# Kernel tuning notes

Measured on AMD Instinct MI355X. Metric: run time of the kernel, lower is better.

Reference implementation:

```python
import jax, jax.numpy as jnp
import numpy as np

B, S, D, H, DH = 2, 1024, 1024, 16, 64  # batch, seq, dim_model, heads, dim_head


def setup_inputs() -> dict:
    key = jax.random.key(0)
    ks = jax.random.split(key, 9)
    def W(k):
        return jax.random.normal(k, (D, D), jnp.float32) * 0.02
    z = jnp.zeros((D,), jnp.float32)
    return {
        "x": jax.random.normal(ks[0], (B, S, D), jnp.float32),
        "rel_pos_emb": jax.random.normal(ks[1], (B, S, D), jnp.float32),
        "padding_mask": jnp.zeros((B, S), jnp.int32),
        "Wq": W(ks[2]), "bq": z,
        "Wk": W(ks[3]), "bk": z,
        "Wv": W(ks[4]), "bv": z,
        "Wqr": W(ks[5]), "bqr": z,
        "Wkr": W(ks[6]), "bkr": z,
        "Wc": W(ks[7]), "bc": z,
    }


def reference(x, rel_pos_emb, padding_mask, Wq, bq, Wk, bk, Wv, bv, Wqr, bqr, Wkr, bkr, Wc, bc):
    b, s, d = x.shape

    def proj(t, W_, b_):  # (b,s,D) -> (b,H,s,DH)
        return (t @ W_.T + b_).reshape(b, s, H, DH).transpose(0, 2, 1, 3)

    q = proj(x, Wq, bq)
    k = proj(x, Wk, bk)
    v = proj(x, Wv, bv)
    qr = proj(rel_pos_emb, Wqr, bqr)
    kr = proj(rel_pos_emb, Wkr, bkr)

    # relative position index: clamp(i - j + MAX_REL_POS/2, 0, MAX_REL_POS-1), MAX_REL_POS = S
    idx = jnp.arange(s)
    pos = jnp.clip(idx[:, None] - idx[None, :] + s // 2, 0, s - 1)  # (s,s) int
    pos_b = jnp.broadcast_to(pos[None, None], (b, H, s, s))

    c2c = jnp.einsum('bhid,bhjd->bhij', q, k)
    c2p_att = jnp.einsum('bhid,bhjd->bhij', q, kr)
    c2p = jnp.take_along_axis(c2p_att, pos_b, axis=-1)   # gather along last dim
    p2c_att = jnp.einsum('bhid,bhjd->bhij', qr, k)
    p2c = jnp.take_along_axis(p2c_att, pos_b, axis=-2)   # gather along query dim

    scale = jnp.sqrt(jnp.asarray(3 * DH, jnp.float32))
    scores = (c2c + c2p + p2c) / scale
    scores = jnp.where(padding_mask[:, None, None, :] == 1, -jnp.inf, scores)
    attn = jax.nn.softmax(scores, axis=-1)  # dropout is identity in eval

    out = jnp.einsum('bhij,bhjd->bhid', attn, v)
    out = out.transpose(0, 2, 1, 3).reshape(b, s, H * DH)
    return out @ Wc.T + bc
```

## Files before the change

### kernel.cpp

```cpp
#include <hip/hip_runtime.h>

typedef unsigned short u16;
typedef unsigned int   u32;
typedef __bf16 bf16x8 __attribute__((ext_vector_type(8)));
typedef float  f32x4  __attribute__((ext_vector_type(4)));

__device__ __forceinline__ float b2f(u16 s) { return __uint_as_float(((u32)s) << 16); }
__device__ __forceinline__ u16 f2b(float f) {
  u32 x = __float_as_uint(f);
  return (u16)((x + 0x7FFFu + ((x >> 16) & 1u)) >> 16);
}

union U16x8 { uint4 u; u16 s[8]; };

__device__ __forceinline__ uint4 cvt8(const float4 a, const float4 b) {
  U16x8 r;
  r.s[0] = f2b(a.x); r.s[1] = f2b(a.y); r.s[2] = f2b(a.z); r.s[3] = f2b(a.w);
  r.s[4] = f2b(b.x); r.s[5] = f2b(b.y); r.s[6] = f2b(b.z); r.s[7] = f2b(b.w);
  return r.u;
}

typedef __attribute__((address_space(3))) u32 lds_u32;
typedef const __attribute__((address_space(1))) u32 glb_u32;
__device__ __forceinline__ void gld16(const u16* gp, u16* lp) {
  __builtin_amdgcn_global_load_lds((glb_u32*)gp, (lds_u32*)lp, 16, 0, 0);
}

struct CvtArgs { const float* s[8]; u16* d[8]; int n[8]; };

__global__ __launch_bounds__(256) void cvt_bf16(CvtArgs c) {
  const int t = blockIdx.y;
  const int i = (blockIdx.x * 256 + threadIdx.x) * 8;
  if (i >= c.n[t]) return;
  const float4 a = *(const float4*)(c.s[t] + i);
  const float4 b = *(const float4*)(c.s[t] + i + 4);
  *(uint4*)(c.d[t] + i) = cvt8(a, b);
}

struct GemmBArgs { const u16* A[5]; const u16* W[5]; const float* Bi[5]; void* C[5]; int vtz; };

template <int BN, bool OUT_F32>
__global__ __launch_bounds__(256) void gemm_lds(GemmBArgs g, int M, int N, int K) {
  const int z = blockIdx.z;
  const u16* __restrict__ A = g.A[z];
  const u16* __restrict__ W = g.W[z];
  const float* __restrict__ Bi = g.Bi[z];

  const int m0 = blockIdx.y * 128, n0 = blockIdx.x * BN;
  const int tid = threadIdx.x, wv = tid >> 6, lane = tid & 63;
  const int wm = wv >> 1, wn = wv & 1;
  const int lr = lane & 15, lq = lane >> 4;
  constexpr int NT = BN / 32;

  __shared__ u16 As[128 * 64];
  __shared__ u16 Ws[BN * 64];

  const f32x4 vzero = {0.f, 0.f, 0.f, 0.f};
  f32x4 acc[4][NT];
#pragma unroll
  for (int i = 0; i < 4; ++i)
#pragma unroll
    for (int j = 0; j < NT; ++j) acc[i][j] = vzero;

  const int srow = lane >> 3;
  const int sc   = (lane & 7) ^ srow;

  for (int kb = 0; kb < K; kb += 64) {
    __syncthreads();
#pragma unroll
    for (int t = 0; t < 4; ++t) {
      const u16* gp = A + (size_t)(m0 + t * 32 + wv * 8 + srow) * K + kb + sc * 8;
      gld16(gp, As + (t * 32 + wv * 8) * 64 + lane * 8);
    }
#pragma unroll
    for (int t = 0; t < NT; ++t) {
      const u16* gp = W + (size_t)(n0 + t * 32 + wv * 8 + srow) * K + kb + sc * 8;
      gld16(gp, Ws + (t * 32 + wv * 8) * 64 + lane * 8);
    }
    __syncthreads();
#pragma unroll
    for (int kk = 0; kk < 2; ++kk) {
      bf16x8 af[4], bw[NT];
#pragma unroll
      for (int mt = 0; mt < 4; ++mt) {
        const int row = wm * 64 + mt * 16 + lr;
        af[mt] = *(const bf16x8*)&As[row * 64 + (((kk << 2) | lq) ^ (row & 7)) * 8];
      }
#pragma unroll
      for (int nt = 0; nt < NT; ++nt) {
        const int row = wn * (BN / 2) + nt * 16 + lr;
        bw[nt] = *(const bf16x8*)&Ws[row * 64 + (((kk << 2) | lq) ^ (row & 7)) * 8];
      }
#pragma unroll
      for (int mt = 0; mt < 4; ++mt)
#pragma unroll
        for (int nt = 0; nt < NT; ++nt)
          acc[mt][nt] = __builtin_amdgcn_mfma_f32_16x16x32_bf16(af[mt], bw[nt], acc[mt][nt], 0, 0, 0);
    }
  }

#pragma unroll
  for (int mt = 0; mt < 4; ++mt) {
#pragma unroll
    for (int nt = 0; nt < NT; ++nt) {
      const int col = n0 + wn * (BN / 2) + nt * 16 + lr;
      const float bia = Bi[col];
      const int row0 = m0 + wm * 64 + mt * 16 + lq * 4;
      if (OUT_F32) {
#pragma unroll
        for (int r = 0; r < 4; ++r)
          ((float*)g.C[z])[(size_t)(row0 + r) * N + col] = acc[mt][nt][r] + bia;
      } else if (z == g.vtz) {
        ushort4 pk;
        pk.x = f2b(acc[mt][nt][0] + bia); pk.y = f2b(acc[mt][nt][1] + bia);
        pk.z = f2b(acc[mt][nt][2] + bia); pk.w = f2b(acc[mt][nt][3] + bia);
        const int bb = row0 >> 10, s0 = row0 & 1023;
        *(ushort4*)((u16*)g.C[z] + ((size_t)bb << 20) + ((size_t)col << 10) + s0) = pk;
      } else {
#pragma unroll
        for (int r = 0; r < 4; ++r)
          ((u16*)g.C[z])[(size_t)(row0 + r) * N + col] = f2b(acc[mt][nt][r] + bia);
      }
    }
  }
}

struct GemmArgs { const void* A[5]; const float* W[5]; const float* Bi[5]; void* C[5]; int vtz; };

template <bool A_F32, bool OUT_F32>
__global__ __launch_bounds__(256) void gemm5(GemmArgs g, int M, int N, int K) {
  const int z = blockIdx.z;
  const float* __restrict__ Wf = g.W[z];
  const float* __restrict__ Bi = g.Bi[z];

  const int m0 = blockIdx.y * 128, n0 = blockIdx.x * 128;
  const int tid = threadIdx.x;
  const int wv = tid >> 6, lane = tid & 63;
  const int wm = wv >> 1, wn = wv & 1;
  const int lr = lane & 15, lq = lane >> 4;

  __shared__ alignas(16) u16 As[128][64];
  __shared__ alignas(16) u16 Ws[128][64];

  const f32x4 vzero = {0.f, 0.f, 0.f, 0.f};
  f32x4 acc[4][4];
#pragma unroll
  for (int i = 0; i < 4; ++i)
#pragma unroll
    for (int j = 0; j < 4; ++j) acc[i][j] = vzero;

  const int srow = tid >> 1;
  const int sc0  = (tid & 1) * 32;
  const float* pw = Wf + (size_t)(n0 + srow) * K + sc0;
  const float* paf = A_F32 ? ((const float*)g.A[z] + (size_t)(m0 + srow) * K + sc0) : nullptr;
  const u16*   pab = A_F32 ? nullptr : ((const u16*)g.A[z] + (size_t)(m0 + srow) * K + sc0);

  for (int k0 = 0; k0 < K; k0 += 64) {
#pragma unroll
    for (int u_ = 0; u_ < 4; ++u_) {
      const float4 w0 = *(const float4*)(pw + k0 + u_ * 8);
      const float4 w1 = *(const float4*)(pw + k0 + u_ * 8 + 4);
      *(uint4*)&Ws[srow][sc0 + u_ * 8] = cvt8(w0, w1);
      if (A_F32) {
        const float4 a0 = *(const float4*)(paf + k0 + u_ * 8);
        const float4 a1 = *(const float4*)(paf + k0 + u_ * 8 + 4);
        *(uint4*)&As[srow][sc0 + u_ * 8] = cvt8(a0, a1);
      } else {
        *(uint4*)&As[srow][sc0 + u_ * 8] = *(const uint4*)(pab + k0 + u_ * 8);
      }
    }
    __syncthreads();
#pragma unroll
    for (int kk = 0; kk < 2; ++kk) {
      bf16x8 af[4], bfr[4];
#pragma unroll
      for (int mt = 0; mt < 4; ++mt)
        af[mt] = *(const bf16x8*)&As[wm * 64 + mt * 16 + lr][kk * 32 + lq * 8];
#pragma unroll
      for (int nt = 0; nt < 4; ++nt)
        bfr[nt] = *(const bf16x8*)&Ws[wn * 64 + nt * 16 + lr][kk * 32 + lq * 8];
#pragma unroll
      for (int mt = 0; mt < 4; ++mt)
#pragma unroll
        for (int nt = 0; nt < 4; ++nt)
          acc[mt][nt] = __builtin_amdgcn_mfma_f32_16x16x32_bf16(af[mt], bfr[nt], acc[mt][nt], 0, 0, 0);
    }
    __syncthreads();
  }

#pragma unroll
  for (int mt = 0; mt < 4; ++mt) {
#pragma unroll
    for (int nt = 0; nt < 4; ++nt) {
      const int col = n0 + wn * 64 + nt * 16 + lr;
      const float bia = Bi[col];
      const int row0 = m0 + wm * 64 + mt * 16 + lq * 4;
      if (OUT_F32) {
#pragma unroll
        for (int r = 0; r < 4; ++r)
          ((float*)g.C[z])[(size_t)(row0 + r) * N + col] = acc[mt][nt][r] + bia;
      } else if (z == g.vtz) {
        ushort4 pk;
        pk.x = f2b(acc[mt][nt][0] + bia); pk.y = f2b(acc[mt][nt][1] + bia);
        pk.z = f2b(acc[mt][nt][2] + bia); pk.w = f2b(acc[mt][nt][3] + bia);
        const int bb = row0 >> 10, s0 = row0 & 1023;
        *(ushort4*)((u16*)g.C[z] + ((size_t)bb << 20) + ((size_t)col << 10) + s0) = pk;
      } else {
#pragma unroll
        for (int r = 0; r < 4; ++r)
          ((u16*)g.C[z])[(size_t)(row0 + r) * N + col] = f2b(acc[mt][nt][r] + bia);
      }
    }
  }
}

__global__ __launch_bounds__(256) void attn_fused(
    const u16* __restrict__ q, const u16* __restrict__ k,
    const u16* __restrict__ vT, const u16* __restrict__ qr,
    const u16* __restrict__ kr, const int* __restrict__ pmask,
    u16* __restrict__ ao) {
  constexpr int S = 1024, Dm = 1024;

  const int bx = blockIdx.x;
  const int bh = bx & 31, it = bx >> 5;
  const int bb = bh >> 4, h = bh & 15;
  const int i0 = it * 32;

  const int tid = threadIdx.x;
  const int wv = tid >> 6, lane = tid & 63;
  const int wm = wv >> 1, wn = wv & 1;
  const int lr = lane & 15, lq = lane >> 4;

  __shared__ alignas(16) u16 Qs[32][72];
  __shared__ alignas(16) u16 Ks[32][72];
  __shared__ alignas(16) u16 Vt[64][40];
  __shared__ alignas(16) u16 KRw[64][72];
  __shared__ alignas(16) u16 QRw[64][72];
  __shared__ alignas(16) float Sc[32][36];
  __shared__ alignas(16) u16 M1s[32][68];
  __shared__ alignas(16) u16 M2s[64][36];
  __shared__ alignas(16) u16 Pb[32][40];
  __shared__ float mrow[32], lrow_[32], arow[32];
  __shared__ int maskj[32];

  const size_t hoff = (size_t)h * 64;
  const u16* qb  = q  + (size_t)bb * S * Dm + hoff;
  const u16* kb  = k  + (size_t)bb * S * Dm + hoff;
  const u16* vtb = vT + ((size_t)bb << 20) + ((size_t)h << 16);
  const u16* qrb = qr + (size_t)bb * S * Dm + hoff;
  const u16* krb = kr + (size_t)bb * S * Dm + hoff;

  if (tid < 32) { mrow[tid] = -1e30f; lrow_[tid] = 0.f; }
  {
    const int a = tid >> 3, seg = (tid & 7) * 8;
    *(uint4*)&Qs[a][seg] = *(const uint4*)(qb + (size_t)(i0 + a) * Dm + seg);
  }

  const f32x4 vzero = {0.f, 0.f, 0.f, 0.f};
  f32x4 oacc[2] = {vzero, vzero};
  const float kscale = 1.44269504088896f / 13.856406460551018f;

#pragma unroll 1
  for (int jt = 0; jt < 32; ++jt) {
    const int j0 = jt * 32;
    const int pb_ = i0 - j0 + 481;
    __syncthreads();

    {
      const int jj = tid >> 3, d0 = (tid & 7) * 8;
      *(uint4*)&Ks[jj][d0] = *(const uint4*)(kb + (size_t)(j0 + jj) * Dm + d0);
      const int d = tid >> 2, jseg = (tid & 3) * 8;
      *(uint4*)&Vt[d][jseg] = *(const uint4*)(vtb + ((size_t)d << 10) + j0 + jseg);
    }
    {
      const int trow = tid >> 2, sg = (tid & 3) * 16;
      int p = pb_ + trow; p = p < 0 ? 0 : (p > 1023 ? 1023 : p);
      const u16* krp = krb + (size_t)p * Dm + sg;
      const u16* qrp = qrb + (size_t)p * Dm + sg;
      *(uint4*)&KRw[trow][sg]     = *(const uint4*)krp;
      *(uint4*)&KRw[trow][sg + 8] = *(const uint4*)(krp + 8);
      *(uint4*)&QRw[trow][sg]     = *(const uint4*)qrp;
      *(uint4*)&QRw[trow][sg + 8] = *(const uint4*)(qrp + 8);
    }
    if (tid < 32) maskj[tid] = pmask[(size_t)bb * S + j0 + tid];
    __syncthreads();

    bf16x8 aq[2], bkf[2];
#pragma unroll
    for (int kk = 0; kk < 2; ++kk) {
      aq[kk]  = *(const bf16x8*)&Qs[wm * 16 + lr][kk * 32 + lq * 8];
      bkf[kk] = *(const bf16x8*)&Ks[wn * 16 + lr][kk * 32 + lq * 8];
    }
    {
      f32x4 cc = vzero;
      cc = __builtin_amdgcn_mfma_f32_16x16x32_bf16(aq[0], bkf[0], cc, 0, 0, 0);
      cc = __builtin_amdgcn_mfma_f32_16x16x32_bf16(aq[1], bkf[1], cc, 0, 0, 0);
#pragma unroll
      for (int r = 0; r < 4; ++r) Sc[wm * 16 + lq * 4 + r][wn * 16 + lr] = cc[r];
    }
#pragma unroll
    for (int nti = 0; nti < 2; ++nti) {
      const int nt = wn + nti * 2;
      f32x4 m1 = vzero;
#pragma unroll
      for (int kk = 0; kk < 2; ++kk) {
        bf16x8 bkr8 = *(const bf16x8*)&KRw[nt * 16 + lr][kk * 32 + lq * 8];
        m1 = __builtin_amdgcn_mfma_f32_16x16x32_bf16(aq[kk], bkr8, m1, 0, 0, 0);
      }
#pragma unroll
      for (int r = 0; r < 4; ++r) M1s[wm * 16 + lq * 4 + r][nt * 16 + lr] = f2b(m1[r]);
    }
#pragma unroll
    for (int mti = 0; mti < 2; ++mti) {
      const int mt = wm + mti * 2;
      f32x4 m2 = vzero;
#pragma unroll
      for (int kk = 0; kk < 2; ++kk) {
        bf16x8 aqr8 = *(const bf16x8*)&QRw[mt * 16 + lr][kk * 32 + lq * 8];
        m2 = __builtin_amdgcn_mfma_f32_16x16x32_bf16(aqr8, bkf[kk], m2, 0, 0, 0);
      }
#pragma unroll
      for (int r = 0; r < 4; ++r) M2s[mt * 16 + lq * 4 + r][wn * 16 + lr] = f2b(m2[r]);
    }
    __syncthreads();

    {
      const int a_ = tid >> 3;
      const int b0 = (tid & 7) * 4;
      const float4 sc4 = *(const float4*)&Sc[a_][b0];
      float sv[4];
      sv[0] = sc4.x; sv[1] = sc4.y; sv[2] = sc4.z; sv[3] = sc4.w;
#pragma unroll
      for (int xq = 0; xq < 4; ++xq) {
        const int b_ = b0 + xq;
        const int tI = a_ - b_ + 31;
        const float scv = sv[xq] + b2f(M1s[a_][tI]) + b2f(M2s[tI][b_]);
        sv[xq] = maskj[b_] ? -1e30f : scv * kscale;
      }
      float mx = fmaxf(fmaxf(sv[0], sv[1]), fmaxf(sv[2], sv[3]));
      mx = fmaxf(mx, __shfl_xor(mx, 1));
      mx = fmaxf(mx, __shfl_xor(mx, 2));
      mx = fmaxf(mx, __shfl_xor(mx, 4));
      const float mold = mrow[a_];
      const float mnew = fmaxf(mold, mx);
      float ls = 0.f;
      u32 pk[2];
#pragma unroll
      for (int xq = 0; xq < 2; ++xq) {
        const float p0 = exp2f(sv[2 * xq] - mnew);
        const float p1 = exp2f(sv[2 * xq + 1] - mnew);
        ls += p0 + p1;
        pk[xq] = (u32)f2b(p0) | ((u32)f2b(p1) << 16);
      }
      ls += __shfl_xor(ls, 1);
      ls += __shfl_xor(ls, 2);
      ls += __shfl_xor(ls, 4);
      if ((tid & 7) == 0) {
        const float al = exp2f(mold - mnew);
        mrow[a_] = mnew;
        lrow_[a_] = lrow_[a_] * al + ls;
        arow[a_] = al;
      }
      *(u32*)&Pb[a_][b0]     = pk[0];
      *(u32*)&Pb[a_][b0 + 2] = pk[1];
    }
    __syncthreads();

    {
      float alph[4];
#pragma unroll
      for (int r = 0; r < 4; ++r) alph[r] = arow[wm * 16 + lq * 4 + r];
#pragma unroll
      for (int t2 = 0; t2 < 2; ++t2)
#pragma unroll
        for (int r = 0; r < 4; ++r) oacc[t2][r] *= alph[r];
      bf16x8 ap = *(const bf16x8*)&Pb[wm * 16 + lr][lq * 8];
#pragma unroll
      for (int nti = 0; nti < 2; ++nti) {
        const int nt = wn + nti * 2;
        bf16x8 bv8 = *(const bf16x8*)&Vt[nt * 16 + lr][lq * 8];
        oacc[nti] = __builtin_amdgcn_mfma_f32_16x16x32_bf16(ap, bv8, oacc[nti], 0, 0, 0);
      }
    }
  }

#pragma unroll
  for (int nti = 0; nti < 2; ++nti) {
    const int nt = wn + nti * 2;
#pragma unroll
    for (int r = 0; r < 4; ++r) {
      const int rl = wm * 16 + lq * 4 + r;
      const float ov = oacc[nti][r] / lrow_[rl];
      ao[((size_t)bb * S + i0 + rl) * Dm + hoff + nt * 16 + lr] = f2b(ov);
    }
  }
}

extern "C" void kernel_launch(void* const* d_in, const int* in_sizes, int n_in,
                              void* d_out, int out_size, void* d_ws, size_t ws_size,
                              hipStream_t stream) {
  const float* x   = (const float*)d_in[0];
  const float* rpe = (const float*)d_in[1];
  const int*   pm  = (const int*)d_in[2];
  const float* Wq  = (const float*)d_in[3];  const float* bq  = (const float*)d_in[4];
  const float* Wk  = (const float*)d_in[5];  const float* bk  = (const float*)d_in[6];
  const float* Wv  = (const float*)d_in[7];  const float* bv  = (const float*)d_in[8];
  const float* Wqr = (const float*)d_in[9];  const float* bqr = (const float*)d_in[10];
  const float* Wkr = (const float*)d_in[11]; const float* bkr = (const float*)d_in[12];
  const float* Wc  = (const float*)d_in[13]; const float* bc  = (const float*)d_in[14];

  const size_t NE = (size_t)2 * 1024 * 1024;
  const size_t WE = (size_t)1024 * 1024;
  u16* ws = (u16*)d_ws;

  if (ws_size >= (10 * NE + 6 * WE) * sizeof(u16)) {
    u16* q   = ws;          u16* k   = ws + NE;     u16* vT  = ws + 2 * NE;
    u16* qr  = ws + 3 * NE; u16* kr  = ws + 4 * NE;
    u16* xb  = ws + 5 * NE;
    u16* ao  = ws + 5 * NE;
    u16* rpb = ws + 6 * NE;
    u16* wb  = ws + 7 * NE;
    u16* Wqb = wb;           u16* Wkb = wb + WE;     u16* Wvb = wb + 2 * WE;
    u16* Wqrb= wb + 3 * WE;  u16* Wkrb= wb + 4 * WE; u16* Wcb = wb + 5 * WE;

    CvtArgs c;
    c.s[0] = x;   c.d[0] = xb;   c.n[0] = (int)NE;
    c.s[1] = rpe; c.d[1] = rpb;  c.n[1] = (int)NE;
    c.s[2] = Wq;  c.d[2] = Wqb;  c.n[2] = (int)WE;
    c.s[3] = Wk;  c.d[3] = Wkb;  c.n[3] = (int)WE;
    c.s[4] = Wv;  c.d[4] = Wvb;  c.n[4] = (int)WE;
    c.s[5] = Wqr; c.d[5] = Wqrb; c.n[5] = (int)WE;
    c.s[6] = Wkr; c.d[6] = Wkrb; c.n[6] = (int)WE;
    c.s[7] = Wc;  c.d[7] = Wcb;  c.n[7] = (int)WE;
    cvt_bf16<<<dim3(1024, 8), 256, 0, stream>>>(c);

    GemmBArgs g;
    g.A[0] = xb;  g.W[0] = Wqb;  g.Bi[0] = bq;  g.C[0] = q;
    g.A[1] = xb;  g.W[1] = Wkb;  g.Bi[1] = bk;  g.C[1] = k;
    g.A[2] = xb;  g.W[2] = Wvb;  g.Bi[2] = bv;  g.C[2] = vT;
    g.A[3] = rpb; g.W[3] = Wqrb; g.Bi[3] = bqr; g.C[3] = qr;
    g.A[4] = rpb; g.W[4] = Wkrb; g.Bi[4] = bkr; g.C[4] = kr;
    g.vtz = 2;
    gemm_lds<128, false><<<dim3(8, 16, 5), 256, 0, stream>>>(g, 2048, 1024, 1024);

    attn_fused<<<dim3(1024), 256, 0, stream>>>(q, k, vT, qr, kr, pm, ao);

    GemmBArgs g2;
    for (int i = 0; i < 5; ++i) { g2.A[i] = ao; g2.W[i] = Wcb; g2.Bi[i] = bc; g2.C[i] = d_out; }
    g2.vtz = -1;
    gemm_lds<64, true><<<dim3(16, 16, 1), 256, 0, stream>>>(g2, 2048, 1024, 1024);
  } else {
    if (ws_size < 6 * NE * sizeof(u16)) return;
    u16* q  = ws;          u16* k  = ws + NE;     u16* vT = ws + 2 * NE;
    u16* qr = ws + 3 * NE; u16* kr = ws + 4 * NE; u16* ao = ws + 5 * NE;

    GemmArgs g;
    g.A[0] = x;   g.W[0] = Wq;  g.Bi[0] = bq;  g.C[0] = q;
    g.A[1] = x;   g.W[1] = Wk;  g.Bi[1] = bk;  g.C[1] = k;
    g.A[2] = x;   g.W[2] = Wv;  g.Bi[2] = bv;  g.C[2] = vT;
    g.A[3] = rpe; g.W[3] = Wqr; g.Bi[3] = bqr; g.C[3] = qr;
    g.A[4] = rpe; g.W[4] = Wkr; g.Bi[4] = bkr; g.C[4] = kr;
    g.vtz = 2;
    gemm5<true, false><<<dim3(8, 16, 5), 256, 0, stream>>>(g, 2048, 1024, 1024);

    attn_fused<<<dim3(1024), 256, 0, stream>>>(q, k, vT, qr, kr, pm, ao);

    GemmArgs g2;
    for (int i = 0; i < 5; ++i) { g2.A[i] = ao; g2.W[i] = Wc; g2.Bi[i] = bc; g2.C[i] = d_out; }
    g2.vtz = -1;
    gemm5<false, true><<<dim3(8, 16, 1), 256, 0, stream>>>(g2, 2048, 1024, 1024);
  }
}
```

Baseline: 288.6 us.

## Split attention KV loop across waves with per-wave softmax and final merge

The attention kernel is restructured so each of the four waves independently handles a quarter of the key tiles for all 32 query rows. Each wave keeps its own online-softmax state in registers and loads K, KR, QR and V fragments straight from global memory into registers. The four partial results are combined once at the end through LDS. This removes the four block-wide barriers per key tile, and the c2p/p2c terms now stay in fp32. In exchange it uses more registers and makes redundant, uncoalesced global loads of Q and QR fragments per wave.

Result: faster. 261.5 us (-9.4%).

```diff
diff --git a/kernel.cpp b/kernel.cpp
--- a/kernel.cpp
+++ b/kernel.cpp
@@ -214,12 +214,17 @@
   }
 }
 
-__global__ __launch_bounds__(256) void attn_fused(
+__global__ __launch_bounds__(256, 2) void attn_wave(
     const u16* __restrict__ q, const u16* __restrict__ k,
     const u16* __restrict__ vT, const u16* __restrict__ qr,
     const u16* __restrict__ kr, const int* __restrict__ pmask,
     u16* __restrict__ ao) {
   constexpr int S = 1024, Dm = 1024;
+  constexpr int GP = 37;
+  constexpr int PBP = 36;
+  constexpr int WLDS = 11776;
+
+  __shared__ alignas(16) char smem[4 * WLDS];
 
   const int bx = blockIdx.x;
   const int bh = bx & 31, it = bx >> 5;
@@ -228,171 +233,222 @@
 
   const int tid = threadIdx.x;
   const int wv = tid >> 6, lane = tid & 63;
-  const int wm = wv >> 1, wn = wv & 1;
-  const int lr = lane & 15, lq = lane >> 4;
-
-  __shared__ alignas(16) u16 Qs[32][72];
-  __shared__ alignas(16) u16 Ks[32][72];
-  __shared__ alignas(16) u16 Vt[64][40];
-  __shared__ alignas(16) u16 KRw[64][72];
-  __shared__ alignas(16) u16 QRw[64][72];
-  __shared__ alignas(16) float Sc[32][36];
-  __shared__ alignas(16) u16 M1s[32][68];
-  __shared__ alignas(16) u16 M2s[64][36];
-  __shared__ alignas(16) u16 Pb[32][40];
-  __shared__ float mrow[32], lrow_[32], arow[32];
-  __shared__ int maskj[32];
-
-  const size_t hoff = (size_t)h * 64;
-  const u16* qb  = q  + (size_t)bb * S * Dm + hoff;
-  const u16* kb  = k  + (size_t)bb * S * Dm + hoff;
+  const int lq = lane >> 4, lr = lane & 15;
+
+  char* wbase = smem + wv * WLDS;
+  float* G1b = (float*)wbase;
+  float* G2b = (float*)(wbase + 4736);
+  u16*   Pb  = (u16*)(wbase + 9472);
+
+  const u16* qb  = q  + ((size_t)bb << 20) + h * 64;
+  const u16* kb  = k  + ((size_t)bb << 20) + h * 64;
+  const u16* qrb = qr + ((size_t)bb << 20) + h * 64;
+  const u16* krb = kr + ((size_t)bb << 20) + h * 64;
   const u16* vtb = vT + ((size_t)bb << 20) + ((size_t)h << 16);
-  const u16* qrb = qr + (size_t)bb * S * Dm + hoff;
-  const u16* krb = kr + (size_t)bb * S * Dm + hoff;
-
-  if (tid < 32) { mrow[tid] = -1e30f; lrow_[tid] = 0.f; }
+  const int* pmb = pmask + ((size_t)bb << 10);
+
+  const float kscale = 1.44269504088896f / 13.856406460551018f;
+
+  bf16x8 qf[2][2];
+#pragma unroll
+  for (int mt = 0; mt < 2; ++mt)
+#pragma unroll
+    for (int kk = 0; kk < 2; ++kk)
+      qf[mt][kk] = *(const bf16x8*)(qb + (size_t)(i0 + mt * 16 + lr) * Dm + kk * 32 + lq * 8);
+
+  const f32x4 vzero = {0.f, 0.f, 0.f, 0.f};
+  f32x4 o[2][4];
+#pragma unroll
+  for (int mt = 0; mt < 2; ++mt)
+#pragma unroll
+    for (int nd = 0; nd < 4; ++nd) o[mt][nd] = vzero;
+  float mst[2][4], lst[2][4];
+#pragma unroll
+  for (int mt = 0; mt < 2; ++mt)
+#pragma unroll
+    for (int r = 0; r < 4; ++r) { mst[mt][r] = -1e30f; lst[mt][r] = 0.f; }
+
+#pragma unroll 1
+  for (int t8 = 0; t8 < 8; ++t8) {
+    const int j0 = (wv + t8 * 4) * 32;
+    const int pb_ = i0 - j0 + 481;
+
+    bf16x8 kf[2][2], krf[4][2], vf[4];
+#pragma unroll
+    for (int nt = 0; nt < 2; ++nt) {
+      const u16* kp = kb + (size_t)(j0 + nt * 16 + lr) * Dm + lq * 8;
+      kf[nt][0] = *(const bf16x8*)kp;
+      kf[nt][1] = *(const bf16x8*)(kp + 32);
+    }
+#pragma unroll
+    for (int n4 = 0; n4 < 4; ++n4) {
+      int p = pb_ + n4 * 16 + lr; p = p < 0 ? 0 : (p > 1023 ? 1023 : p);
+      const u16* kp = krb + (size_t)p * Dm + lq * 8;
+      krf[n4][0] = *(const bf16x8*)kp;
+      krf[n4][1] = *(const bf16x8*)(kp + 32);
+    }
+#pragma unroll
+    for (int n4 = 0; n4 < 4; ++n4)
+      vf[n4] = *(const bf16x8*)(vtb + (size_t)(n4 * 16 + lr) * S + j0 + lq * 8);
+    const int mv0 = pmb[j0 + lr], mv1 = pmb[j0 + 16 + lr];
+
+    f32x4 cc[2][2];
+#pragma unroll
+    for (int mt = 0; mt < 2; ++mt)
+#pragma unroll
+      for (int nt = 0; nt < 2; ++nt) {
+        f32x4 a = vzero;
+        a = __builtin_amdgcn_mfma_f32_16x16x32_bf16(qf[mt][0], kf[nt][0], a, 0, 0, 0);
+        a = __builtin_amdgcn_mfma_f32_16x16x32_bf16(qf[mt][1], kf[nt][1], a, 0, 0, 0);
+        cc[mt][nt] = a;
+      }
+
+#pragma unroll
+    for (int mt = 0; mt < 2; ++mt)
+#pragma unroll
+      for (int n4 = 0; n4 < 4; ++n4) {
+        f32x4 a = vzero;
+        a = __builtin_amdgcn_mfma_f32_16x16x32_bf16(qf[mt][0], krf[n4][0], a, 0, 0, 0);
+        a = __builtin_amdgcn_mfma_f32_16x16x32_bf16(qf[mt][1], krf[n4][1], a, 0, 0, 0);
+        const int t = n4 * 16 + lr;
+#pragma unroll
+        for (int r = 0; r < 4; ++r) {
+          const int arow = mt * 16 + lq * 4 + r;
+          const int u = t - arow;
+          if ((unsigned)u < 32u) G1b[arow * GP + u] = a[r];
+        }
+      }
+
+#pragma unroll
+    for (int mt = 0; mt < 2; ++mt)
+#pragma unroll
+      for (int n4 = 0; n4 < 4; ++n4) {
+        int p = pb_ + n4 * 16 + lr; p = p < 0 ? 0 : (p > 1023 ? 1023 : p);
+        const u16* qp = qrb + (size_t)p * Dm + lq * 8;
+        bf16x8 q0 = *(const bf16x8*)qp;
+        bf16x8 q1 = *(const bf16x8*)(qp + 32);
+        f32x4 a = vzero;
+        a = __builtin_amdgcn_mfma_f32_16x16x32_bf16(kf[mt][0], q0, a, 0, 0, 0);
+        a = __builtin_amdgcn_mfma_f32_16x16x32_bf16(kf[mt][1], q1, a, 0, 0, 0);
+        const int t = n4 * 16 + lr;
+#pragma unroll
+        for (int r = 0; r < 4; ++r) {
+          const int brow = mt * 16 + lq * 4 + r;
+          const int u = t + brow - 31;
+          if ((unsigned)u < 32u) G2b[brow * GP + u] = a[r];
+        }
+      }
+
+    float pv[2][2][4], alpha[2][4];
+#pragma unroll
+    for (int mt = 0; mt < 2; ++mt) {
+      float mx[4];
+#pragma unroll
+      for (int r = 0; r < 4; ++r) {
+        const int a_ = mt * 16 + lq * 4 + r;
+#pragma unroll
+        for (int nt = 0; nt < 2; ++nt) {
+          const int b_ = nt * 16 + lr;
+          float s = cc[mt][nt][r] + G1b[a_ * GP + 31 - b_] + G2b[b_ * GP + a_];
+          s *= kscale;
+          if ((nt ? mv1 : mv0) != 0) s = -1e30f;
+          pv[mt][nt][r] = s;
+        }
+        mx[r] = fmaxf(pv[mt][0][r], pv[mt][1][r]);
+      }
+#pragma unroll
+      for (int r = 0; r < 4; ++r) {
+        mx[r] = fmaxf(mx[r], __shfl_xor(mx[r], 1));
+        mx[r] = fmaxf(mx[r], __shfl_xor(mx[r], 2));
+        mx[r] = fmaxf(mx[r], __shfl_xor(mx[r], 4));
+        mx[r] = fmaxf(mx[r], __shfl_xor(mx[r], 8));
+        const float mnew = fmaxf(mst[mt][r], mx[r]);
+        alpha[mt][r] = exp2f(mst[mt][r] - mnew);
+        mst[mt][r] = mnew;
+        float rs = 0.f;
+#pragma unroll
+        for (int nt = 0; nt < 2; ++nt) {
+          const float p = exp2f(pv[mt][nt][r] - mnew);
+          pv[mt][nt][r] = p;
+          rs += p;
+        }
+        rs += __shfl_xor(rs, 1);
+        rs += __shfl_xor(rs, 2);
+        rs += __shfl_xor(rs, 4);
+        rs += __shfl_xor(rs, 8);
+        lst[mt][r] = lst[mt][r] * alpha[mt][r] + rs;
+        const int a_ = mt * 16 + lq * 4 + r;
+#pragma unroll
+        for (int nt = 0; nt < 2; ++nt)
+          Pb[a_ * PBP + nt * 16 + lr] = f2b(pv[mt][nt][r]);
+      }
+    }
+
+#pragma unroll
+    for (int mt = 0; mt < 2; ++mt)
+#pragma unroll
+      for (int nd = 0; nd < 4; ++nd)
+#pragma unroll
+        for (int r = 0; r < 4; ++r) o[mt][nd][r] *= alpha[mt][r];
+#pragma unroll
+    for (int mt = 0; mt < 2; ++mt) {
+      union { uint2 u2[2]; bf16x8 v; } pr;
+      const u16* prow = Pb + (mt * 16 + lr) * PBP + lq * 8;
+      pr.u2[0] = *(const uint2*)prow;
+      pr.u2[1] = *(const uint2*)(prow + 4);
+#pragma unroll
+      for (int nd = 0; nd < 4; ++nd)
+        o[mt][nd] = __builtin_amdgcn_mfma_f32_16x16x32_bf16(pr.v, vf[nd], o[mt][nd], 0, 0, 0);
+    }
+  }
+
   {
-    const int a = tid >> 3, seg = (tid & 7) * 8;
-    *(uint4*)&Qs[a][seg] = *(const uint4*)(qb + (size_t)(i0 + a) * Dm + seg);
-  }
-
-  const f32x4 vzero = {0.f, 0.f, 0.f, 0.f};
-  f32x4 oacc[2] = {vzero, vzero};
-  const float kscale = 1.44269504088896f / 13.856406460551018f;
-
-#pragma unroll 1
-  for (int jt = 0; jt < 32; ++jt) {
-    const int j0 = jt * 32;
-    const int pb_ = i0 - j0 + 481;
-    __syncthreads();
-
-    {
-      const int jj = tid >> 3, d0 = (tid & 7) * 8;
-      *(uint4*)&Ks[jj][d0] = *(const uint4*)(kb + (size_t)(j0 + jj) * Dm + d0);
-      const int d = tid >> 2, jseg = (tid & 3) * 8;
-      *(uint4*)&Vt[d][jseg] = *(const uint4*)(vtb + ((size_t)d << 10) + j0 + jseg);
-    }
-    {
-      const int trow = tid >> 2, sg = (tid & 3) * 16;
-      int p = pb_ + trow; p = p < 0 ? 0 : (p > 1023 ? 1023 : p);
-      const u16* krp = krb + (size_t)p * Dm + sg;
-      const u16* qrp = qrb + (size_t)p * Dm + sg;
-      *(uint4*)&KRw[trow][sg]     = *(const uint4*)krp;
-      *(uint4*)&KRw[trow][sg + 8] = *(const uint4*)(krp + 8);
-      *(uint4*)&QRw[trow][sg]     = *(const uint4*)qrp;
-      *(uint4*)&QRw[trow][sg + 8] = *(const uint4*)(qrp + 8);
-    }
-    if (tid < 32) maskj[tid] = pmask[(size_t)bb * S + j0 + tid];
-    __syncthreads();
-
-    bf16x8 aq[2], bkf[2];
-#pragma unroll
-    for (int kk = 0; kk < 2; ++kk) {
-      aq[kk]  = *(const bf16x8*)&Qs[wm * 16 + lr][kk * 32 + lq * 8];
-      bkf[kk] = *(const bf16x8*)&Ks[wn * 16 + lr][kk * 32 + lq * 8];
-    }
-    {
-      f32x4 cc = vzero;
-      cc = __builtin_amdgcn_mfma_f32_16x16x32_bf16(aq[0], bkf[0], cc, 0, 0, 0);
-      cc = __builtin_amdgcn_mfma_f32_16x16x32_bf16(aq[1], bkf[1], cc, 0, 0, 0);
-#pragma unroll
-      for (int r = 0; r < 4; ++r) Sc[wm * 16 + lq * 4 + r][wn * 16 + lr] = cc[r];
-    }
-#pragma unroll
-    for (int nti = 0; nti < 2; ++nti) {
-      const int nt = wn + nti * 2;
-      f32x4 m1 = vzero;
-#pragma unroll
-      for (int kk = 0; kk < 2; ++kk) {
-        bf16x8 bkr8 = *(const bf16x8*)&KRw[nt * 16 + lr][kk * 32 + lq * 8];
-        m1 = __builtin_amdgcn_mfma_f32_16x16x32_bf16(aq[kk], bkr8, m1, 0, 0, 0);
-      }
-#pragma unroll
-      for (int r = 0; r < 4; ++r) M1s[wm * 16 + lq * 4 + r][nt * 16 + lr] = f2b(m1[r]);
-    }
-#pragma unroll
-    for (int mti = 0; mti < 2; ++mti) {
-      const int mt = wm + mti * 2;
-      f32x4 m2 = vzero;
-#pragma unroll
-      for (int kk = 0; kk < 2; ++kk) {
-        bf16x8 aqr8 = *(const bf16x8*)&QRw[mt * 16 + lr][kk * 32 + lq * 8];
-        m2 = __builtin_amdgcn_mfma_f32_16x16x32_bf16(aqr8, bkf[kk], m2, 0, 0, 0);
-      }
-#pragma unroll
-      for (int r = 0; r < 4; ++r) M2s[mt * 16 + lq * 4 + r][wn * 16 + lr] = f2b(m2[r]);
-    }
-    __syncthreads();
-
-    {
-      const int a_ = tid >> 3;
-      const int b0 = (tid & 7) * 4;
-      const float4 sc4 = *(const float4*)&Sc[a_][b0];
-      float sv[4];
-      sv[0] = sc4.x; sv[1] = sc4.y; sv[2] = sc4.z; sv[3] = sc4.w;
-#pragma unroll
-      for (int xq = 0; xq < 4; ++xq) {
-        const int b_ = b0 + xq;
-        const int tI = a_ - b_ + 31;
-        const float scv = sv[xq] + b2f(M1s[a_][tI]) + b2f(M2s[tI][b_]);
-        sv[xq] = maskj[b_] ? -1e30f : scv * kscale;
-      }
-      float mx = fmaxf(fmaxf(sv[0], sv[1]), fmaxf(sv[2], sv[3]));
-      mx = fmaxf(mx, __shfl_xor(mx, 1));
-      mx = fmaxf(mx, __shfl_xor(mx, 2));
-      mx = fmaxf(mx, __shfl_xor(mx, 4));
-      const float mold = mrow[a_];
-      const float mnew = fmaxf(mold, mx);
-      float ls = 0.f;
-      u32 pk[2];
-#pragma unroll
-      for (int xq = 0; xq < 2; ++xq) {
-        const float p0 = exp2f(sv[2 * xq] - mnew);
-        const float p1 = exp2f(sv[2 * xq + 1] - mnew);
-        ls += p0 + p1;
-        pk[xq] = (u32)f2b(p0) | ((u32)f2b(p1) << 16);
-      }
-      ls += __shfl_xor(ls, 1);
-      ls += __shfl_xor(ls, 2);
-      ls += __shfl_xor(ls, 4);
-      if ((tid & 7) == 0) {
-        const float al = exp2f(mold - mnew);
-        mrow[a_] = mnew;
-        lrow_[a_] = lrow_[a_] * al + ls;
-        arow[a_] = al;
-      }
-      *(u32*)&Pb[a_][b0]     = pk[0];
-      *(u32*)&Pb[a_][b0 + 2] = pk[1];
-    }
-    __syncthreads();
-
-    {
-      float alph[4];
-#pragma unroll
-      for (int r = 0; r < 4; ++r) alph[r] = arow[wm * 16 + lq * 4 + r];
-#pragma unroll
-      for (int t2 = 0; t2 < 2; ++t2)
-#pragma unroll
-        for (int r = 0; r < 4; ++r) oacc[t2][r] *= alph[r];
-      bf16x8 ap = *(const bf16x8*)&Pb[wm * 16 + lr][lq * 8];
-#pragma unroll
-      for (int nti = 0; nti < 2; ++nti) {
-        const int nt = wn + nti * 2;
-        bf16x8 bv8 = *(const bf16x8*)&Vt[nt * 16 + lr][lq * 8];
-        oacc[nti] = __builtin_amdgcn_mfma_f32_16x16x32_bf16(ap, bv8, oacc[nti], 0, 0, 0);
-      }
-    }
-  }
-
-#pragma unroll
-  for (int nti = 0; nti < 2; ++nti) {
-    const int nt = wn + nti * 2;
-#pragma unroll
-    for (int r = 0; r < 4; ++r) {
-      const int rl = wm * 16 + lq * 4 + r;
-      const float ov = oacc[nti][r] / lrow_[rl];
-      ao[((size_t)bb * S + i0 + rl) * Dm + hoff + nt * 16 + lr] = f2b(ov);
-    }
+    float* Orm = (float*)wbase;
+    float* mlw = (float*)(wbase + 8192);
+    float* llw = (float*)(wbase + 8320);
+#pragma unroll
+    for (int mt = 0; mt < 2; ++mt)
+#pragma unroll
+      for (int nd = 0; nd < 4; ++nd)
+#pragma unroll
+        for (int r = 0; r < 4; ++r)
+          Orm[(mt * 16 + lq * 4 + r) * 64 + nd * 16 + lr] = o[mt][nd][r];
+    if (lr == 0) {
+#pragma unroll
+      for (int mt = 0; mt < 2; ++mt)
+#pragma unroll
+        for (int r = 0; r < 4; ++r) {
+          mlw[mt * 16 + lq * 4 + r] = mst[mt][r];
+          llw[mt * 16 + lq * 4 + r] = lst[mt][r];
+        }
+    }
+  }
+  __syncthreads();
+  {
+    const int a_ = tid >> 3, d0 = (tid & 7) * 8;
+    float Ms = -1e30f;
+#pragma unroll
+    for (int w = 0; w < 4; ++w)
+      Ms = fmaxf(Ms, *(const float*)(smem + w * WLDS + 8192 + a_ * 4));
+    float L = 0.f, acc[8];
+#pragma unroll
+    for (int d = 0; d < 8; ++d) acc[d] = 0.f;
+#pragma unroll
+    for (int w = 0; w < 4; ++w) {
+      const char* wb = smem + w * WLDS;
+      const float mw = *(const float*)(wb + 8192 + a_ * 4);
+      const float lw = *(const float*)(wb + 8320 + a_ * 4);
+      const float al = exp2f(mw - Ms);
+      L += al * lw;
+      const float* Ow = (const float*)wb + a_ * 64 + d0;
+#pragma unroll
+      for (int d = 0; d < 8; ++d) acc[d] += al * Ow[d];
+    }
+    const float inv = 1.f / L;
+    U16x8 pk;
+#pragma unroll
+    for (int d = 0; d < 8; ++d) pk.s[d] = f2b(acc[d] * inv);
+    *(uint4*)(ao + ((size_t)((bb << 10) + i0 + a_) << 10) + (h << 6) + d0) = pk.u;
   }
 }
 
@@ -443,7 +499,7 @@
     g.vtz = 2;
     gemm_lds<128, false><<<dim3(8, 16, 5), 256, 0, stream>>>(g, 2048, 1024, 1024);
 
-    attn_fused<<<dim3(1024), 256, 0, stream>>>(q, k, vT, qr, kr, pm, ao);
+    attn_wave<<<dim3(1024), 256, 0, stream>>>(q, k, vT, qr, kr, pm, ao);
 
     GemmBArgs g2;
     for (int i = 0; i < 5; ++i) { g2.A[i] = ao; g2.W[i] = Wcb; g2.Bi[i] = bc; g2.C[i] = d_out; }
@@ -463,7 +519,7 @@
     g.vtz = 2;
     gemm5<true, false><<<dim3(8, 16, 5), 256, 0, stream>>>(g, 2048, 1024, 1024);
 
-    attn_fused<<<dim3(1024), 256, 0, stream>>>(q, k, vT, qr, kr, pm, ao);
+    attn_wave<<<dim3(1024), 256, 0, stream>>>(q, k, vT, qr, kr, pm, ao);
 
     GemmArgs g2;
     for (int i = 0; i < 5; ++i) { g2.A[i] = ao; g2.W[i] = Wc; g2.Bi[i] = bc; g2.C[i] = d_out; }
```
